# Kernel optimization log

Measured on AMD Instinct MI355X. Metric: run time of the kernel, lower is better.

## Reference

```python
import jax, jax.numpy as jnp
import numpy as np

EPS = 1e-4          # ReEig epsilon buffer
IN_SIZE = 4096      # input SPD matrix is IN_SIZE x IN_SIZE
HID = 5             # hard-coded bottleneck in RiemSPD
OUT_SIZE = 2048     # output SPD matrix is OUT_SIZE x OUT_SIZE


def _orthogonal(key, rows, cols):
    # mimic nn.init.orthogonal_: semi-orthogonal (rows, cols) matrix
    n, m = max(rows, cols), min(rows, cols)
    a = jax.random.normal(key, (n, m), dtype=jnp.float32)
    q, _ = jnp.linalg.qr(a)
    q = q[:, :m]
    return q if rows >= cols else q.T


def bimap(x, w):
    # BiMap.forward: W^T @ X @ W
    return w.T @ (x @ w)


def rectify(x):
    # Rectify.forward: SVD, clip singular values at EPS, rebuild u diag(s) u^T
    u, s, _ = jnp.linalg.svd(x)
    s = jnp.maximum(s, EPS)
    return (u * s[None, :]) @ u.T


def setup_inputs() -> dict:
    key = jax.random.key(0)
    k1, k2, k3 = jax.random.split(key, 3)
    X = jax.random.normal(k1, (1, IN_SIZE, IN_SIZE), dtype=jnp.float32)
    W1 = _orthogonal(k2, IN_SIZE, HID)   # encoder BiMap weight (in_size, 5)
    W2 = _orthogonal(k3, HID, OUT_SIZE)  # decoder BiMap weight (5, out_size)
    return {"X": X, "W1": W1, "W2": W2}


def reference(X, W1, W2):
    x = X[0]                       # squeeze(0): (IN_SIZE, IN_SIZE)
    y = rectify(bimap(x, W1))      # encoder: (5, 5)
    z = rectify(bimap(y, W2))      # decoder: (OUT_SIZE, OUT_SIZE)
    return z
```

## Files before the change

kernel.cpp:

```cpp
#include <hip/hip_runtime.h>
#include <math.h>

static constexpr int N   = 4096;
static constexpr int H   = 5;
static constexpr int NO  = 2048;
static constexpr float FEPS = 1e-4f;
static constexpr int NJC  = 4;
static constexpr int NIG  = 128;
static constexpr int RPB  = N / NIG;
static constexpr int NBLK = NIG * NJC;
static constexpr int NCON = 256;
static constexpr int NR   = NO / NCON;

#if __has_builtin(__builtin_amdgcn_rcpf)
__device__ __forceinline__ float frcp(float x) { return __builtin_amdgcn_rcpf(x); }
#else
__device__ __forceinline__ float frcp(float x) { return 1.0f / x; }
#endif
#if __has_builtin(__builtin_amdgcn_rsqf)
__device__ __forceinline__ float frsq(float x) { return __builtin_amdgcn_rsqf(x); }
#else
__device__ __forceinline__ float frsq(float x) { return 1.0f / sqrtf(x); }
#endif

__device__ __forceinline__ float wave_reduce(float v) {
#pragma unroll
    for (int o = 32; o > 0; o >>= 1) v += __shfl_down(v, o, 64);
    return v;
}

__global__ __launch_bounds__(256) void k_xw1(const float* __restrict__ X,
                                             const float* __restrict__ W1,
                                             float* __restrict__ Mp) {
    const int b   = blockIdx.x;
    const int ig  = b >> 2;
    const int jcb = b & 3;
    const int t   = threadIdx.x;
    const int j4  = jcb * 256 + t;
    const float4* W14 = reinterpret_cast<const float4*>(W1);

    float wf[20];
    {
        const float4 f0 = W14[5 * j4 + 0];
        const float4 f1 = W14[5 * j4 + 1];
        const float4 f2 = W14[5 * j4 + 2];
        const float4 f3 = W14[5 * j4 + 3];
        const float4 f4 = W14[5 * j4 + 4];
        wf[0]=f0.x;  wf[1]=f0.y;  wf[2]=f0.z;  wf[3]=f0.w;
        wf[4]=f1.x;  wf[5]=f1.y;  wf[6]=f1.z;  wf[7]=f1.w;
        wf[8]=f2.x;  wf[9]=f2.y;  wf[10]=f2.z; wf[11]=f2.w;
        wf[12]=f3.x; wf[13]=f3.y; wf[14]=f3.z; wf[15]=f3.w;
        wf[16]=f4.x; wf[17]=f4.y; wf[18]=f4.z; wf[19]=f4.w;
    }

    float pm[H][H];
#pragma unroll
    for (int a = 0; a < H; ++a)
#pragma unroll
        for (int bb = 0; bb < H; ++bb) pm[a][bb] = 0.f;

    const int i0 = ig * RPB;
#pragma unroll 4
    for (int r = 0; r < RPB; ++r) {
        const float4 x = reinterpret_cast<const float4*>(
                             X + (size_t)(i0 + r) * N)[j4];
        float t5[H];
#pragma unroll
        for (int a = 0; a < H; ++a)
            t5[a] = x.x * wf[a]      + x.y * wf[5 + a]
                  + x.z * wf[10 + a] + x.w * wf[15 + a];
        float w1r[H];
#pragma unroll
        for (int a = 0; a < H; ++a) w1r[a] = W1[(size_t)(i0 + r) * H + a];
#pragma unroll
        for (int a = 0; a < H; ++a)
#pragma unroll
            for (int bb = 0; bb < H; ++bb) pm[a][bb] += w1r[a] * t5[bb];
    }

    __shared__ float sm[4][25];
    {
        const int lane = t & 63, wv = t >> 6;
#pragma unroll
        for (int a = 0; a < H; ++a)
#pragma unroll
            for (int bb = 0; bb < H; ++bb) {
                const float v = wave_reduce(pm[a][bb]);
                if (lane == 0) sm[wv][a * H + bb] = v;
            }
    }
    __syncthreads();
    if (t < 25)
        Mp[b * 25 + t] = sm[0][t] + sm[1][t] + sm[2][t] + sm[3][t];
}

#define JROT(p, q)                                                            \
    {                                                                         \
        const float apq = __shfl(a, (p) * 5 + (q), 64);                       \
        const float app = __shfl(a, (p) * 5 + (p), 64);                       \
        const float aqq = __shfl(a, (q) * 5 + (q), 64);                       \
        const bool  skip =                                                    \
            (apq * apq) <= (1e-26f * (app * app + aqq * aqq) + 1e-38f);       \
        const float theta = (aqq - app) * frcp(2.0f * apq);                   \
        const float tden  = fabsf(theta) + sqrtf(theta * theta + 1.0f);       \
        const float ttv   = ((theta >= 0.0f) ? 1.0f : -1.0f) * frcp(tden);    \
        float cc = frsq(ttv * ttv + 1.0f);                                    \
        float ss = ttv * cc;                                                  \
        cc = skip ? 1.0f : cc;                                                \
        ss = skip ? 0.0f : ss;                                                \
        {                                                                     \
            const int  pr   = ((r == (p)) ? (q) : ((r == (q)) ? (p) : r));    \
            const float prt = __shfl(a, pr * 5 + c, 64);                      \
            a = (r == (p)) ? (cc * a - ss * prt)                              \
                           : ((r == (q)) ? (ss * prt + cc * a) : a);          \
        }                                                                     \
        {                                                                     \
            const int  pc   = ((c == (p)) ? (q) : ((c == (q)) ? (p) : c));    \
            const float prt = __shfl(a, r * 5 + pc, 64);                      \
            a = (c == (p)) ? (cc * a - ss * prt)                              \
                           : ((c == (q)) ? (ss * prt + cc * a) : a);          \
            const float urt = __shfl(u, r * 5 + pc, 64);                      \
            u = (c == (p)) ? (cc * u - ss * urt)                              \
                           : ((c == (q)) ? (ss * urt + cc * u) : u);          \
        }                                                                     \
    }

__global__ __launch_bounds__(256) void k_out(const float* __restrict__ Mp,
                                             const float* __restrict__ W2,
                                             float* __restrict__ Z) {
    __shared__ float sred[10][26];
    __shared__ float Msum[25];
    __shared__ float ys[25];
    const int t = threadIdx.x;

    if (t < 250) {
        const int e = t % 25, g = t / 25;
        float s = 0.f;
#pragma unroll 8
        for (int p = g; p < NBLK; p += 10) s += Mp[p * 25 + e];
        sred[g][e] = s;
    }
    __syncthreads();
    if (t < 25) {
        float s = 0.f;
#pragma unroll
        for (int g = 0; g < 10; ++g) s += sred[g][t];
        Msum[t] = s;
    }
    __syncthreads();

    if (t < 64) {
        const int r = t / 5, c = t % 5;
        const float m = (t < 25) ? Msum[t] : 0.f;
        float a = 0.f;
#pragma unroll
        for (int k = 0; k < H; ++k)
            a += __shfl(m, r * 5 + k, 64) * __shfl(m, c * 5 + k, 64);
        float u = (t < 25 && r == c) ? 1.0f : 0.0f;

        for (int sweep = 0; sweep < 6; ++sweep) {
            JROT(0, 1) JROT(0, 2) JROT(0, 3) JROT(0, 4) JROT(1, 2)
            JROT(1, 3) JROT(1, 4) JROT(2, 3) JROT(2, 4) JROT(3, 4)
        }

        const float ev = fmaxf(sqrtf(fmaxf(a, 0.0f)), FEPS);
        float yv = 0.f;
#pragma unroll
        for (int k = 0; k < H; ++k) {
            const float evk = __shfl(ev, 6 * k, 64);
            const float urk = __shfl(u, r * 5 + k, 64);
            const float uck = __shfl(u, c * 5 + k, 64);
            yv += evk * urk * uck;
        }
        if (t < 25) ys[t] = yv - ((r == c) ? FEPS : 0.f);
    }
    __syncthreads();

    const int i0 = blockIdx.x * NR;
    float cmat[NR][H];
#pragma unroll
    for (int r = 0; r < NR; ++r) {
        float wcol[H];
#pragma unroll
        for (int k = 0; k < H; ++k) wcol[k] = W2[(size_t)k * NO + i0 + r];
#pragma unroll
        for (int m = 0; m < H; ++m) {
            float s = 0.f;
#pragma unroll
            for (int k = 0; k < H; ++k) s += wcol[k] * ys[k * H + m];
            cmat[r][m] = s;
        }
    }

#pragma unroll
    for (int hh = 0; hh < 2; ++hh) {
        const int jj = (hh * 256 + t) * 4;
        float4 w2j[H];
#pragma unroll
        for (int m = 0; m < H; ++m)
            w2j[m] = *reinterpret_cast<const float4*>(W2 + (size_t)m * NO + jj);
#pragma unroll
        for (int r = 0; r < NR; ++r) {
            const int i = i0 + r;
            float zx = 0.f, zy = 0.f, zz = 0.f, zw = 0.f;
#pragma unroll
            for (int m = 0; m < H; ++m) {
                const float cm = cmat[r][m];
                zx += cm * w2j[m].x;
                zy += cm * w2j[m].y;
                zz += cm * w2j[m].z;
                zw += cm * w2j[m].w;
            }
            if (i >= jj && i < jj + 4) {
                if      (i == jj + 0) zx += FEPS;
                else if (i == jj + 1) zy += FEPS;
                else if (i == jj + 2) zz += FEPS;
                else                  zw += FEPS;
            }
            *reinterpret_cast<float4*>(Z + (size_t)i * NO + jj) =
                make_float4(zx, zy, zz, zw);
        }
    }
}

extern "C" void kernel_launch(void* const* d_in, const int* in_sizes, int n_in,
                              void* d_out, int out_size, void* d_ws, size_t ws_size,
                              hipStream_t stream) {
    const float* X  = (const float*)d_in[0];
    const float* W1 = (const float*)d_in[1];
    const float* W2 = (const float*)d_in[2];
    float* out = (float*)d_out;
    float* ws  = (float*)d_ws;

    float* Mp = ws;

    hipLaunchKernelGGL(k_xw1, dim3(NBLK), dim3(256), 0, stream, X, W1, Mp);
    hipLaunchKernelGGL(k_out, dim3(NCON), dim3(256), 0, stream, Mp, W2, out);
}
```

Measured before the change: 41.04 us.

## Move partial reduction and 5x5 eigensolve into last-finishing block of first kernel

Uses an atomic completion counter so the last block of the X·W1 kernel sums all partials and runs the Jacobi eigen-decomposition once, writing the 25-element rectified matrix to workspace. Previously every one of the 256 output blocks redundantly reduced 512x25 partials and ran the eigensolver before writing its slice of Z. The change removes that per-block serial prologue from the output kernel. In exchange it adds a memset launch, an atomic counter and relaxed atomic loads and stores with no explicit fence, which may carry memory-ordering risk.

```diff
diff --git a/kernel.cpp b/kernel.cpp
--- a/kernel.cpp
+++ b/kernel.cpp
@@ -27,71 +27,6 @@
 #pragma unroll
     for (int o = 32; o > 0; o >>= 1) v += __shfl_down(v, o, 64);
     return v;
-}
-
-__global__ __launch_bounds__(256) void k_xw1(const float* __restrict__ X,
-                                             const float* __restrict__ W1,
-                                             float* __restrict__ Mp) {
-    const int b   = blockIdx.x;
-    const int ig  = b >> 2;
-    const int jcb = b & 3;
-    const int t   = threadIdx.x;
-    const int j4  = jcb * 256 + t;
-    const float4* W14 = reinterpret_cast<const float4*>(W1);
-
-    float wf[20];
-    {
-        const float4 f0 = W14[5 * j4 + 0];
-        const float4 f1 = W14[5 * j4 + 1];
-        const float4 f2 = W14[5 * j4 + 2];
-        const float4 f3 = W14[5 * j4 + 3];
-        const float4 f4 = W14[5 * j4 + 4];
-        wf[0]=f0.x;  wf[1]=f0.y;  wf[2]=f0.z;  wf[3]=f0.w;
-        wf[4]=f1.x;  wf[5]=f1.y;  wf[6]=f1.z;  wf[7]=f1.w;
-        wf[8]=f2.x;  wf[9]=f2.y;  wf[10]=f2.z; wf[11]=f2.w;
-        wf[12]=f3.x; wf[13]=f3.y; wf[14]=f3.z; wf[15]=f3.w;
-        wf[16]=f4.x; wf[17]=f4.y; wf[18]=f4.z; wf[19]=f4.w;
-    }
-
-    float pm[H][H];
-#pragma unroll
-    for (int a = 0; a < H; ++a)
-#pragma unroll
-        for (int bb = 0; bb < H; ++bb) pm[a][bb] = 0.f;
-
-    const int i0 = ig * RPB;
-#pragma unroll 4
-    for (int r = 0; r < RPB; ++r) {
-        const float4 x = reinterpret_cast<const float4*>(
-                             X + (size_t)(i0 + r) * N)[j4];
-        float t5[H];
-#pragma unroll
-        for (int a = 0; a < H; ++a)
-            t5[a] = x.x * wf[a]      + x.y * wf[5 + a]
-                  + x.z * wf[10 + a] + x.w * wf[15 + a];
-        float w1r[H];
-#pragma unroll
-        for (int a = 0; a < H; ++a) w1r[a] = W1[(size_t)(i0 + r) * H + a];
-#pragma unroll
-        for (int a = 0; a < H; ++a)
-#pragma unroll
-            for (int bb = 0; bb < H; ++bb) pm[a][bb] += w1r[a] * t5[bb];
-    }
-
-    __shared__ float sm[4][25];
-    {
-        const int lane = t & 63, wv = t >> 6;
-#pragma unroll
-        for (int a = 0; a < H; ++a)
-#pragma unroll
-            for (int bb = 0; bb < H; ++bb) {
-                const float v = wave_reduce(pm[a][bb]);
-                if (lane == 0) sm[wv][a * H + bb] = v;
-            }
-    }
-    __syncthreads();
-    if (t < 25)
-        Mp[b * 25 + t] = sm[0][t] + sm[1][t] + sm[2][t] + sm[3][t];
 }
 
 #define JROT(p, q)                                                            \
@@ -125,19 +60,94 @@
         }                                                                     \
     }
 
-__global__ __launch_bounds__(256) void k_out(const float* __restrict__ Mp,
-                                             const float* __restrict__ W2,
-                                             float* __restrict__ Z) {
+__global__ __launch_bounds__(256) void k_xw1(const float* __restrict__ X,
+                                             const float* __restrict__ W1,
+                                             float* __restrict__ Mp,
+                                             float* __restrict__ ysw,
+                                             unsigned int* __restrict__ done) {
+    const int b   = blockIdx.x;
+    const int ig  = b >> 2;
+    const int jcb = b & 3;
+    const int t   = threadIdx.x;
+    const int j4  = jcb * 256 + t;
+    const float4* W14 = reinterpret_cast<const float4*>(W1);
+
+    float wf[20];
+    {
+        const float4 f0 = W14[5 * j4 + 0];
+        const float4 f1 = W14[5 * j4 + 1];
+        const float4 f2 = W14[5 * j4 + 2];
+        const float4 f3 = W14[5 * j4 + 3];
+        const float4 f4 = W14[5 * j4 + 4];
+        wf[0]=f0.x;  wf[1]=f0.y;  wf[2]=f0.z;  wf[3]=f0.w;
+        wf[4]=f1.x;  wf[5]=f1.y;  wf[6]=f1.z;  wf[7]=f1.w;
+        wf[8]=f2.x;  wf[9]=f2.y;  wf[10]=f2.z; wf[11]=f2.w;
+        wf[12]=f3.x; wf[13]=f3.y; wf[14]=f3.z; wf[15]=f3.w;
+        wf[16]=f4.x; wf[17]=f4.y; wf[18]=f4.z; wf[19]=f4.w;
+    }
+
+    float pm[H][H];
+#pragma unroll
+    for (int a = 0; a < H; ++a)
+#pragma unroll
+        for (int bb = 0; bb < H; ++bb) pm[a][bb] = 0.f;
+
+    const int i0 = ig * RPB;
+#pragma unroll 4
+    for (int r = 0; r < RPB; ++r) {
+        const float4 x = reinterpret_cast<const float4*>(
+                             X + (size_t)(i0 + r) * N)[j4];
+        float t5[H];
+#pragma unroll
+        for (int a = 0; a < H; ++a)
+            t5[a] = x.x * wf[a]      + x.y * wf[5 + a]
+                  + x.z * wf[10 + a] + x.w * wf[15 + a];
+        float w1r[H];
+#pragma unroll
+        for (int a = 0; a < H; ++a) w1r[a] = W1[(size_t)(i0 + r) * H + a];
+#pragma unroll
+        for (int a = 0; a < H; ++a)
+#pragma unroll
+            for (int bb = 0; bb < H; ++bb) pm[a][bb] += w1r[a] * t5[bb];
+    }
+
+    __shared__ float sm[4][25];
+    __shared__ unsigned int lastflag;
+    {
+        const int lane = t & 63, wv = t >> 6;
+#pragma unroll
+        for (int a = 0; a < H; ++a)
+#pragma unroll
+            for (int bb = 0; bb < H; ++bb) {
+                const float v = wave_reduce(pm[a][bb]);
+                if (lane == 0) sm[wv][a * H + bb] = v;
+            }
+    }
+    __syncthreads();
+    if (t < 25) {
+        const float v = sm[0][t] + sm[1][t] + sm[2][t] + sm[3][t];
+        __hip_atomic_store(&Mp[b * 25 + t], v, __ATOMIC_RELAXED,
+                           __HIP_MEMORY_SCOPE_AGENT);
+    }
+    __syncthreads();
+    if (t == 0) {
+        const unsigned int prev =
+            __hip_atomic_fetch_add(done, 1u, __ATOMIC_RELAXED,
+                                   __HIP_MEMORY_SCOPE_AGENT);
+        lastflag = (prev == (unsigned)(NBLK - 1)) ? 1u : 0u;
+    }
+    __syncthreads();
+    if (lastflag == 0) return;
+
     __shared__ float sred[10][26];
     __shared__ float Msum[25];
-    __shared__ float ys[25];
-    const int t = threadIdx.x;
-
     if (t < 250) {
         const int e = t % 25, g = t / 25;
         float s = 0.f;
 #pragma unroll 8
-        for (int p = g; p < NBLK; p += 10) s += Mp[p * 25 + e];
+        for (int p = g; p < NBLK; p += 10)
+            s += __hip_atomic_load(&Mp[p * 25 + e], __ATOMIC_RELAXED,
+                                   __HIP_MEMORY_SCOPE_AGENT);
         sred[g][e] = s;
     }
     __syncthreads();
@@ -172,8 +182,16 @@
             const float uck = __shfl(u, c * 5 + k, 64);
             yv += evk * urk * uck;
         }
-        if (t < 25) ys[t] = yv - ((r == c) ? FEPS : 0.f);
-    }
+        if (t < 25) ysw[t] = yv - ((r == c) ? FEPS : 0.f);
+    }
+}
+
+__global__ __launch_bounds__(256) void k_out(const float* __restrict__ ysw,
+                                             const float* __restrict__ W2,
+                                             float* __restrict__ Z) {
+    __shared__ float ys[25];
+    const int t = threadIdx.x;
+    if (t < 25) ys[t] = ysw[t];
     __syncthreads();
 
     const int i0 = blockIdx.x * NR;
@@ -232,8 +250,12 @@
     float* out = (float*)d_out;
     float* ws  = (float*)d_ws;
 
-    float* Mp = ws;
-
-    hipLaunchKernelGGL(k_xw1, dim3(NBLK), dim3(256), 0, stream, X, W1, Mp);
-    hipLaunchKernelGGL(k_out, dim3(NCON), dim3(256), 0, stream, Mp, W2, out);
-}
+    float* Mp  = ws;
+    float* ysw = ws + NBLK * 25;
+    unsigned int* done = (unsigned int*)(ws + NBLK * 25 + 32);
+
+    (void)hipMemsetAsync(done, 0, sizeof(unsigned int), stream);
+    hipLaunchKernelGGL(k_xw1, dim3(NBLK), dim3(256), 0, stream,
+                       X, W1, Mp, ysw, done);
+    hipLaunchKernelGGL(k_out, dim3(NCON), dim3(256), 0, stream, ysw, W2, out);
+}
```

New measurement: 49.64 us. 20.9% more time.
